# Performance work log

Hardware: AMD Instinct MI355X
Metric: run time of the kernel (lower is better)

The kernel has to match this reference:

```python
import jax, jax.numpy as jnp
import numpy as np
import math

B, N, D = 128, 64, 2
H, M, L = 64, 64, 2
OMEGA = 1.0


def setup_inputs() -> dict:
    key = jax.random.key(0)
    ks = jax.random.split(key, 32)
    s = 0.1  # param scale
    rn = lambda k, shp: jax.random.normal(k, shp, dtype=jnp.float32) * s
    inp = {
        "x": jax.random.normal(ks[0], (B, N, D), dtype=jnp.float32),
        "spin": jnp.zeros((B, N, 1), jnp.float32),
        "node_w1": rn(ks[1], (D + 1, H)), "node_b1": rn(ks[2], (H,)),
        "node_w2": rn(ks[3], (H, H)), "node_b2": rn(ks[4], (H,)),
        "edge_w1": rn(ks[5], (D + 2, M)), "edge_b1": rn(ks[6], (M,)),
        "edge_w2": rn(ks[7], (M, M)), "edge_b2": rn(ks[8], (M,)),
        "v2e_w1": rn(ks[9], (L, H + M, M)), "v2e_b1": rn(ks[10], (L, M)),
        "v2e_w2": rn(ks[11], (L, M, M)), "v2e_b2": rn(ks[12], (L, M)),
        "e2v_w1": rn(ks[13], (L, M, H)), "e2v_b1": rn(ks[14], (L, H)),
        "e2v_w2": rn(ks[15], (L, H, H)), "e2v_b2": rn(ks[16], (L, H)),
        "head_w1": rn(ks[17], (H, H)), "head_b1": rn(ks[18], (H,)),
        "head_w2": rn(ks[19], (H, D)), "head_b2": rn(ks[20], (D,)),
        # bf_scale_init=0.3 -> softplus-inverse
        "scale": jnp.array([math.log(math.exp(0.3) - 1.0)], jnp.float32),
    }
    return inp


def _mlp(x, w1, b1, w2, b2, act):
    return act(x @ w1 + b1) @ w2 + b2


def reference(x, spin, node_w1, node_b1, node_w2, node_b2,
              edge_w1, edge_b1, edge_w2, edge_b2,
              v2e_w1, v2e_b1, v2e_w2, v2e_b2,
              e2v_w1, e2v_b1, e2v_w2, e2v_b2,
              head_w1, head_b1, head_w2, head_b2, scale):
    gelu = lambda t: jax.nn.gelu(t, approximate=False)  # torch exact GELU
    b, n, d = x.shape
    xs = x * jnp.float32(math.sqrt(OMEGA))
    # node embedding: [B,N,H]
    hv = _mlp(jnp.concatenate([xs, spin], -1), node_w1, node_b1, node_w2, node_b2, gelu)
    # dense pairwise edge features; dr[b,i,j] = xs[b,j] - xs[b,i]
    dr = xs[:, None, :, :] - xs[:, :, None, :]            # [B,N,N,D]
    r2 = jnp.sum(dr * dr, axis=-1, keepdims=True)          # [B,N,N,1]
    rr = jnp.sqrt(r2 + 1e-12)
    he = _mlp(jnp.concatenate([dr, rr, r2], -1), edge_w1, edge_b1, edge_w2, edge_b2, gelu)  # [B,N,N,M]
    # mask excludes self-edges (i==j) from aggregation (they were never created
    # in the original edge list; their dense entries never influence off-diag values)
    mask = (1.0 - jnp.eye(n, dtype=x.dtype))[None, :, :, None]
    inv = jnp.float32(1.0 / max(n - 1, 1))
    for l in range(v2e_w1.shape[0]):
        hvb = jnp.broadcast_to(hv[:, :, None, :], (b, n, n, hv.shape[-1]))  # source node i
        he = _mlp(jnp.concatenate([hvb, he], -1), v2e_w1[l], v2e_b1[l], v2e_w2[l], v2e_b2[l], gelu)
        m = _mlp(he, e2v_w1[l], e2v_b1[l], e2v_w2[l], e2v_b2[l], gelu)      # [B,N,N,H]
        hv = hv + jnp.sum(m * mask, axis=1) * inv           # scatter-add over sources i into j
    dx = _mlp(hv, head_w1, head_b1, head_w2, head_b2, jnp.tanh) * jax.nn.softplus(scale[0])
    return dx - jnp.mean(dx, axis=1, keepdims=True)
```

## Files before the change

kernel.cpp:

```cpp
#include <hip/hip_runtime.h>
#include <math.h>


typedef unsigned short u16;
typedef unsigned int u32;
typedef _Float16 half8 __attribute__((ext_vector_type(8)));
typedef __attribute__((ext_vector_type(4))) float floatx4;

#define TS 72

__device__ __forceinline__ float gelu_f(float x) {
    float u = x * 0.70710678118654752f;
    float s = fabsf(u);
    float t = __builtin_amdgcn_rcpf(fmaf(0.3275911f, s, 1.0f));
    float P = t * fmaf(t, fmaf(t, fmaf(t, fmaf(t, 1.061405429f, -1.453152027f),
                                        1.421413741f), -0.284496736f), 0.254829592f);
    float r = copysignf(fmaf(-P, __expf(-s * s), 1.0f), u);
    return 0.5f * x * (1.0f + r);
}

__global__ __launch_bounds__(256) void k_pre1(
    const float* __restrict__ ew2, const float* __restrict__ w1he0,
    const float* __restrict__ w2_0, const float* __restrict__ u1_0,
    const float* __restrict__ w1he1, const float* __restrict__ w2_1,
    const float* __restrict__ u1_1,
    const float* __restrict__ eb2, const float* __restrict__ b2_0,
    const float* __restrict__ c1_0, const float* __restrict__ b2_1,
    const float* __restrict__ c1_1,
    const float* __restrict__ u2_0, const float* __restrict__ u2_1,
    const float* __restrict__ w1n, const float* __restrict__ hw1,
    _Float16* __restrict__ WF,
    float* __restrict__ biasA, float* __restrict__ biasB,
    float* __restrict__ biasC, float* __restrict__ biasD,
    float* __restrict__ u2_0T, float* __restrict__ u2_1T,
    float* __restrict__ w1nT, float* __restrict__ hw1T)
{
    int blk = blockIdx.x;
    if (blk < 64) {
        int s = blk >> 4;
        int idx = (blk & 15) * 256 + threadIdx.x;
        int k = idx >> 6, n = idx & 63;
        const float *A, *Bm;
        if (s == 0)      { A = ew2;  Bm = w1he0; }
        else if (s == 1) { A = w2_0; Bm = u1_0;  }
        else if (s == 2) { A = w2_0; Bm = w1he1; }
        else             { A = w2_1; Bm = u1_1;  }
        float acc = 0.f;
        for (int q = 0; q < 64; ++q) acc = fmaf(A[k * 64 + q], Bm[q * 64 + n], acc);
        int kc = k >> 5, qd = (k >> 3) & 3, jj = k & 7;
        WF[(((s * 2 + kc) * 64 + n) * 4 + qd) * 8 + jj] = (_Float16)acc;
    } else if (blk == 64) {
        int s = threadIdx.x >> 6, cc = threadIdx.x & 63;
        const float *bv, *Bm, *add; float* dst;
        if (s == 0)      { bv = eb2;  Bm = w1he0; add = nullptr; dst = biasA; }
        else if (s == 1) { bv = b2_0; Bm = u1_0;  add = c1_0;    dst = biasB; }
        else if (s == 2) { bv = b2_0; Bm = w1he1; add = nullptr; dst = biasC; }
        else             { bv = b2_1; Bm = u1_1;  add = c1_1;    dst = biasD; }
        float acc = add ? add[cc] : 0.f;
        for (int q = 0; q < 64; ++q) acc = fmaf(bv[q], Bm[q * 64 + cc], acc);
        dst[cc] = acc;
    } else {
        int idx = (blk - 65) * 256 + threadIdx.x;
        int s = idx >> 12, r = idx & 4095, m = r >> 6, tc = r & 63;
        const float* W = s == 0 ? u2_0 : s == 1 ? u2_1 : s == 2 ? w1n : hw1;
        float* WT      = s == 0 ? u2_0T : s == 1 ? u2_1T : s == 2 ? w1nT : hw1T;
        WT[tc * 64 + m] = W[m * 64 + tc];
    }
}

__global__ __launch_bounds__(256) void k_pre2(
    const float* __restrict__ x, const float* __restrict__ spin,
    const float* __restrict__ nw1, const float* __restrict__ nb1,
    const float* __restrict__ nw2, const float* __restrict__ nb2,
    const float* __restrict__ w1_0, const float* __restrict__ b1_0,
    const float* __restrict__ biasA,
    float* __restrict__ hv, float* __restrict__ p0)
{
    __shared__ float a[4][64];
    __shared__ float shv[4][64];
    int w = threadIdx.x >> 6, h = threadIdx.x & 63;
    int node = blockIdx.x * 4 + w;
    float2 xv = ((const float2*)x)[node];
    float sp = spin[node];
    float z = fmaf(xv.x, nw1[h], fmaf(xv.y, nw1[64 + h], fmaf(sp, nw1[128 + h], nb1[h])));
    a[w][h] = gelu_f(z);
    float acc = nb2[h];
    for (int k = 0; k < 64; ++k) acc = fmaf(a[w][k], nw2[k * 64 + h], acc);
    hv[node * 64 + h] = acc;
    shv[w][h] = acc;
    float pa = b1_0[h] + biasA[h];
    for (int k = 0; k < 64; ++k) pa = fmaf(shv[w][k], w1_0[k * 64 + h], pa);
    p0[node * 64 + h] = pa;
}

__device__ __forceinline__ void mfma_acc(
    const _Float16* __restrict__ tA, const _Float16* __restrict__ WF,
    int stage, int c, int quad, int nn, floatx4 acc[4])
{
    int sA = ((nn >> 2) & 3) << 3;
    #pragma unroll
    for (int kc = 0; kc < 2; ++kc) {
        half8 bf = *(const half8*)(WF + (((stage * 2 + kc) * 64 + c) * 4 + quad) * 8);
        int k0 = (kc * 32 + quad * 8) ^ sA;
        #pragma unroll
        for (int mt = 0; mt < 4; ++mt) {
            half8 af = *(const half8*)(tA + (mt * 16 + nn) * TS + k0);
            acc[mt] = __builtin_amdgcn_mfma_f32_16x16x32_f16(af, bf, acc[mt], 0, 0, 0);
        }
    }
}

__device__ __forceinline__ void init_bias(floatx4 acc[4], float bc) {
    #pragma unroll
    for (int mt = 0; mt < 4; ++mt) acc[mt] = (floatx4){bc, bc, bc, bc};
}
__device__ __forceinline__ void init_p(floatx4 acc[4], const float* __restrict__ p,
                                       int rowbase, int c, int quad) {
    #pragma unroll
    for (int mt = 0; mt < 4; ++mt)
        #pragma unroll
        for (int r = 0; r < 4; ++r)
            acc[mt][r] = p[(rowbase + mt * 16 + quad * 4 + r) * 64 + c];
}

__global__ __launch_bounds__(256, 8) void k_L0(
    const float* __restrict__ x,
    const float* __restrict__ ew1, const float* __restrict__ eb1,
    const float* __restrict__ p0,
    const float* __restrict__ biasB,
    const float* __restrict__ u2_0T, const float* __restrict__ c2_0,
    const _Float16* __restrict__ WF,
    const float* __restrict__ hv0, float* __restrict__ hv1,
    const float* __restrict__ w1nT, const float* __restrict__ b1n,
    const float* __restrict__ biasC,
    float* __restrict__ p1,
    u16* __restrict__ he0g)
{
    __shared__ __align__(16) _Float16 tA[64 * TS];
    __shared__ float sgeo[256];
    __shared__ float sS[64];
    __shared__ float shv[64];
    int t = threadIdx.x, w = t >> 6, L = t & 63;
    int nn = L & 15, quad = L >> 4;
    int c = w * 16 + nn;
    int cw = c ^ (quad << 3);
    int b = blockIdx.x >> 6, j = blockIdx.x & 63;

    if (t < 64) {
        float2 xi = ((const float2*)x)[b * 64 + t];
        float2 xj = ((const float2*)x)[b * 64 + j];
        float d0 = xj.x - xi.x, d1 = xj.y - xi.y;
        float r2 = fmaf(d0, d0, d1 * d1);
        sgeo[t] = d0; sgeo[64 + t] = d1; sgeo[128 + t] = sqrtf(r2 + 1e-12f); sgeo[192 + t] = r2;
    }
    __syncthreads();
    {
        int m = t & 63, i0 = t >> 6;
        float wa = ew1[m], wb = ew1[64 + m], wc = ew1[128 + m], wd = ew1[192 + m], bm = eb1[m];
        #pragma unroll
        for (int k = 0; k < 16; ++k) {
            int i = i0 + k * 4;
            float z = fmaf(sgeo[i], wa, fmaf(sgeo[64 + i], wb,
                      fmaf(sgeo[128 + i], wc, fmaf(sgeo[192 + i], wd, bm))));
            tA[i * TS + (m ^ (((i >> 2) & 3) << 3))] = (_Float16)gelu_f(z);
        }
    }
    __syncthreads();

    floatx4 acc[4];
    init_p(acc, p0, b * 64, c, quad);
    mfma_acc(tA, WF, 0, c, quad, nn, acc);
    __syncthreads();
    {
        u16* dst = he0g + (size_t)blockIdx.x * 4096;
        #pragma unroll
        for (int mt = 0; mt < 4; ++mt)
            #pragma unroll
            for (int r = 0; r < 4; ++r) {
                int i = mt * 16 + quad * 4 + r;
                _Float16 y = (_Float16)gelu_f(acc[mt][r]);
                tA[i * TS + cw] = y;
                dst[i * 64 + cw] = __builtin_bit_cast(u16, y);
            }
    }
    __syncthreads();
    init_bias(acc, biasB[c]);
    mfma_acc(tA, WF, 1, c, quad, nn, acc);
    {
        float s = 0.f;
        #pragma unroll
        for (int mt = 0; mt < 4; ++mt)
            #pragma unroll
            for (int r = 0; r < 4; ++r) {
                int i = mt * 16 + quad * 4 + r;
                float g = gelu_f(acc[mt][r]);
                s += (i == j) ? 0.f : g;
            }
        s += __shfl_xor(s, 16);
        s += __shfl_xor(s, 32);
        if (quad == 0) sS[c] = s;
    }
    __syncthreads();
    if (t < 64) {
        const float4* sv4 = (const float4*)sS;
        const float4* uv4 = (const float4*)(u2_0T + t * 64);
        float g = 0.f;
        #pragma unroll
        for (int m4 = 0; m4 < 16; ++m4) {
            float4 sv = sv4[m4], uv = uv4[m4];
            g = fmaf(sv.x, uv.x, fmaf(sv.y, uv.y, fmaf(sv.z, uv.z, fmaf(sv.w, uv.w, g))));
        }
        int o = blockIdx.x * 64 + t;
        float hvv = hv0[o] + g * (1.0f / 63.0f) + c2_0[t];
        hv1[o] = hvv;
        shv[t] = hvv;
        const float4* hv4 = (const float4*)shv;
        const float4* wv4 = (const float4*)(w1nT + t * 64);
        float pa = b1n[t] + biasC[t];
        #pragma unroll
        for (int m4 = 0; m4 < 16; ++m4) {
            float4 sv = hv4[m4], uv = wv4[m4];
            pa = fmaf(sv.x, uv.x, fmaf(sv.y, uv.y, fmaf(sv.z, uv.z, fmaf(sv.w, uv.w, pa))));
        }
        p1[o] = pa;
    }
}

__global__ __launch_bounds__(256, 8) void k_L1(
    const u16* __restrict__ he0g,
    const float* __restrict__ p1,
    const float* __restrict__ biasD,
    const float* __restrict__ u2_1T, const float* __restrict__ c2_1,
    const _Float16* __restrict__ WF,
    const float* __restrict__ hv1,
    const float* __restrict__ hw1T, const float* __restrict__ hb1,
    const float* __restrict__ hw2, const float* __restrict__ hb2,
    const float* __restrict__ scale, float* __restrict__ dx)
{
    __shared__ __align__(16) _Float16 tA[64 * TS];
    __shared__ float sS[64];
    __shared__ float shv[64];
    int t = threadIdx.x, w = t >> 6, L = t & 63;
    int nn = L & 15, quad = L >> 4;
    int c = w * 16 + nn;
    int cw = c ^ (quad << 3);
    int b = blockIdx.x >> 6, j = blockIdx.x & 63;

    {
        const u32* src = (const u32*)(he0g + (size_t)blockIdx.x * 4096);
        for (int qq = t; qq < 2048; qq += 256) {
            u32 v = src[qq];
            int i = qq >> 5, m2 = (qq & 31) * 2;
            *(u32*)((u16*)tA + i * TS + m2) = v;
        }
    }
    __syncthreads();

    floatx4 acc[4];
    init_p(acc, p1, b * 64, c, quad);
    mfma_acc(tA, WF, 2, c, quad, nn, acc);
    __syncthreads();
    #pragma unroll
    for (int mt = 0; mt < 4; ++mt)
        #pragma unroll
        for (int r = 0; r < 4; ++r)
            tA[(mt * 16 + quad * 4 + r) * TS + cw] = (_Float16)gelu_f(acc[mt][r]);
    __syncthreads();
    init_bias(acc, biasD[c]);
    mfma_acc(tA, WF, 3, c, quad, nn, acc);
    {
        float s = 0.f;
        #pragma unroll
        for (int mt = 0; mt < 4; ++mt)
            #pragma unroll
            for (int r = 0; r < 4; ++r) {
                int i = mt * 16 + quad * 4 + r;
                float g = gelu_f(acc[mt][r]);
                s += (i == j) ? 0.f : g;
            }
        s += __shfl_xor(s, 16);
        s += __shfl_xor(s, 32);
        if (quad == 0) sS[c] = s;
    }
    __syncthreads();
    if (t < 64) {
        const float4* sv4 = (const float4*)sS;
        const float4* uv4 = (const float4*)(u2_1T + t * 64);
        float g = 0.f;
        #pragma unroll
        for (int m4 = 0; m4 < 16; ++m4) {
            float4 sv = sv4[m4], uv = uv4[m4];
            g = fmaf(sv.x, uv.x, fmaf(sv.y, uv.y, fmaf(sv.z, uv.z, fmaf(sv.w, uv.w, g))));
        }
        float hv2 = hv1[blockIdx.x * 64 + t] + g * (1.0f / 63.0f) + c2_1[t];
        shv[t] = hv2;
        const float4* hv4 = (const float4*)shv;
        const float4* wv4 = (const float4*)(hw1T + t * 64);
        float a = hb1[t];
        #pragma unroll
        for (int m4 = 0; m4 < 16; ++m4) {
            float4 sv = hv4[m4], uv = wv4[m4];
            a = fmaf(sv.x, uv.x, fmaf(sv.y, uv.y, fmaf(sv.z, uv.z, fmaf(sv.w, uv.w, a))));
        }
        float t1 = tanhf(a);
        float d0 = t1 * hw2[t * 2], d1 = t1 * hw2[t * 2 + 1];
        #pragma unroll
        for (int off = 1; off <= 32; off <<= 1) { d0 += __shfl_xor(d0, off); d1 += __shfl_xor(d1, off); }
        if (t == 0) {
            float sp = log1pf(__expf(scale[0]));
            dx[blockIdx.x * 2 + 0] = (d0 + hb2[0]) * sp;
            dx[blockIdx.x * 2 + 1] = (d1 + hb2[1]) * sp;
        }
    }
}

__global__ __launch_bounds__(64) void k_mean(
    const float* __restrict__ dx, float* __restrict__ out)
{
    __shared__ float s0[64], s1[64];
    int b = blockIdx.x, j = threadIdx.x;
    float2 d = ((const float2*)dx)[b * 64 + j];
    s0[j] = d.x; s1[j] = d.y;
    __syncthreads();
    float m0 = 0.f, m1 = 0.f;
    for (int q = 0; q < 64; ++q) { m0 += s0[q]; m1 += s1[q]; }
    ((float2*)out)[b * 64 + j] = make_float2(d.x - m0 * (1.0f / 64.0f), d.y - m1 * (1.0f / 64.0f));
}

__global__ void k_beacon(float* out, float code) { out[0] = code; }

extern "C" void kernel_launch(void* const* d_in, const int* in_sizes, int n_in,
                              void* d_out, int out_size, void* d_ws, size_t ws_size,
                              hipStream_t stream)
{
    static const int exp_sizes[23] = {
        16384, 8192, 192, 64, 4096, 64,
        256, 64, 4096, 64,
        16384, 128, 8192, 128,
        8192, 128, 8192, 128,
        4096, 64, 128, 2, 1
    };
    float* hv0 = (float*)d_ws;
    float* hv1 = hv0 + 524288;
    float* p0  = hv1 + 524288;
    float* p1  = p0  + 524288;
    float* dx  = p1  + 524288;
    float* u2_0T = dx + 16384;
    float* u2_1T = u2_0T + 4096;
    float* w1nT  = u2_1T + 4096;
    float* hw1T  = w1nT + 4096;
    float* biasA = hw1T + 4096;
    float* biasB = biasA + 64;
    float* biasC = biasB + 64;
    float* biasD = biasC + 64;
    _Float16* WF = (_Float16*)(biasD + 64);
    u16* he0g  = (u16*)(WF + 16384);
    const size_t need = (size_t)((char*)(he0g + 33554432) - (char*)d_ws);

    int bad = -1;
    if (n_in != 23 || out_size != 16384) bad = 98;
    else if (ws_size < need) bad = 97;
    else for (int i = 0; i < 23; ++i)
        if (in_sizes[i] != exp_sizes[i]) { bad = i; break; }
    if (bad >= 0) {
        k_beacon<<<1, 1, 0, stream>>>((float*)d_out, 2e6f + bad * 1e4f);
        return;
    }

    const float* x      = (const float*)d_in[0];
    const float* spin   = (const float*)d_in[1];
    const float* nw1    = (const float*)d_in[2];
    const float* nb1    = (const float*)d_in[3];
    const float* nw2    = (const float*)d_in[4];
    const float* nb2    = (const float*)d_in[5];
    const float* ew1    = (const float*)d_in[6];
    const float* eb1    = (const float*)d_in[7];
    const float* ew2    = (const float*)d_in[8];
    const float* eb2    = (const float*)d_in[9];
    const float* v2e_w1 = (const float*)d_in[10];
    const float* v2e_b1 = (const float*)d_in[11];
    const float* v2e_w2 = (const float*)d_in[12];
    const float* v2e_b2 = (const float*)d_in[13];
    const float* e2v_w1 = (const float*)d_in[14];
    const float* e2v_b1 = (const float*)d_in[15];
    const float* e2v_w2 = (const float*)d_in[16];
    const float* e2v_b2 = (const float*)d_in[17];
    const float* hw1    = (const float*)d_in[18];
    const float* hb1    = (const float*)d_in[19];
    const float* hw2    = (const float*)d_in[20];
    const float* hb2    = (const float*)d_in[21];
    const float* scale  = (const float*)d_in[22];

    k_pre1<<<129, 256, 0, stream>>>(
        ew2, v2e_w1 + 4096, v2e_w2, e2v_w1,
        v2e_w1 + 12288, v2e_w2 + 4096, e2v_w1 + 4096,
        eb2, v2e_b2, e2v_b1, v2e_b2 + 64, e2v_b1 + 64,
        e2v_w2, e2v_w2 + 4096, v2e_w1 + 8192, hw1,
        WF, biasA, biasB, biasC, biasD,
        u2_0T, u2_1T, w1nT, hw1T);
    k_pre2<<<2048, 256, 0, stream>>>(x, spin, nw1, nb1, nw2, nb2,
                                     v2e_w1, v2e_b1, biasA, hv0, p0);
    k_L0<<<8192, 256, 0, stream>>>(x, ew1, eb1,
        p0, biasB, u2_0T, e2v_b2,
        WF, hv0, hv1,
        w1nT, v2e_b1 + 64, biasC, p1,
        he0g);
    k_L1<<<8192, 256, 0, stream>>>(he0g,
        p1, biasD, u2_1T, e2v_b2 + 64,
        WF, hv1, hw1T, hb1, hw2, hb2, scale, dx);
    k_mean<<<128, 64, 0, stream>>>(dx, (float*)d_out);
}
```

Before: 243.6 us.

## Use cheaper erf approximation, spread small matvecs across all waves, pad edge buffer

Swaps the 5-term Abramowitz-Stegun erf polynomial inside GELU for a 3-term version with lower accuracy. Spreads the per-block 64x64 matvecs (message aggregation, next-layer projection, head) across all four wavefronts with a shared-memory reduction, where only one wave did them before. Pads the fp16 edge intermediate to a 72-element row stride so k_L1 can copy it to LDS with 16-byte vector loads. Also builds the first edge-MLP layer per lane with packed half8 stores and no separate geometry staging pass, and folds v2e biases into the precomputed bias vectors. The cheaper erf adds error (about 2.5e-5 absolute), and the split matvecs add extra barriers.

```diff
diff --git a/kernel.cpp b/kernel.cpp
--- a/kernel.cpp
+++ b/kernel.cpp
@@ -8,13 +8,14 @@
 typedef __attribute__((ext_vector_type(4))) float floatx4;
 
 #define TS 72
+#define HROW 72
+#define HBLK (64 * HROW)
 
 __device__ __forceinline__ float gelu_f(float x) {
     float u = x * 0.70710678118654752f;
     float s = fabsf(u);
-    float t = __builtin_amdgcn_rcpf(fmaf(0.3275911f, s, 1.0f));
-    float P = t * fmaf(t, fmaf(t, fmaf(t, fmaf(t, 1.061405429f, -1.453152027f),
-                                        1.421413741f), -0.284496736f), 0.254829592f);
+    float t = __builtin_amdgcn_rcpf(fmaf(0.47047f, s, 1.0f));
+    float P = t * fmaf(t, fmaf(t, 0.7478556f, -0.0958798f), 0.3480242f);
     float r = copysignf(fmaf(-P, __expf(-s * s), 1.0f), u);
     return 0.5f * x * (1.0f + r);
 }
@@ -27,6 +28,7 @@
     const float* __restrict__ eb2, const float* __restrict__ b2_0,
     const float* __restrict__ c1_0, const float* __restrict__ b2_1,
     const float* __restrict__ c1_1,
+    const float* __restrict__ b1_0v, const float* __restrict__ b1nv,
     const float* __restrict__ u2_0, const float* __restrict__ u2_1,
     const float* __restrict__ w1n, const float* __restrict__ hw1,
     _Float16* __restrict__ WF,
@@ -52,11 +54,11 @@
     } else if (blk == 64) {
         int s = threadIdx.x >> 6, cc = threadIdx.x & 63;
         const float *bv, *Bm, *add; float* dst;
-        if (s == 0)      { bv = eb2;  Bm = w1he0; add = nullptr; dst = biasA; }
-        else if (s == 1) { bv = b2_0; Bm = u1_0;  add = c1_0;    dst = biasB; }
-        else if (s == 2) { bv = b2_0; Bm = w1he1; add = nullptr; dst = biasC; }
-        else             { bv = b2_1; Bm = u1_1;  add = c1_1;    dst = biasD; }
-        float acc = add ? add[cc] : 0.f;
+        if (s == 0)      { bv = eb2;  Bm = w1he0; add = b1_0v; dst = biasA; }
+        else if (s == 1) { bv = b2_0; Bm = u1_0;  add = c1_0;  dst = biasB; }
+        else if (s == 2) { bv = b2_0; Bm = w1he1; add = b1nv;  dst = biasC; }
+        else             { bv = b2_1; Bm = u1_1;  add = c1_1;  dst = biasD; }
+        float acc = add[cc];
         for (int q = 0; q < 64; ++q) acc = fmaf(bv[q], Bm[q * 64 + cc], acc);
         dst[cc] = acc;
     } else {
@@ -72,7 +74,7 @@
     const float* __restrict__ x, const float* __restrict__ spin,
     const float* __restrict__ nw1, const float* __restrict__ nb1,
     const float* __restrict__ nw2, const float* __restrict__ nb2,
-    const float* __restrict__ w1_0, const float* __restrict__ b1_0,
+    const float* __restrict__ w1_0,
     const float* __restrict__ biasA,
     float* __restrict__ hv, float* __restrict__ p0)
 {
@@ -88,7 +90,7 @@
     for (int k = 0; k < 64; ++k) acc = fmaf(a[w][k], nw2[k * 64 + h], acc);
     hv[node * 64 + h] = acc;
     shv[w][h] = acc;
-    float pa = b1_0[h] + biasA[h];
+    float pa = biasA[h];
     for (int k = 0; k < 64; ++k) pa = fmaf(shv[w][k], w1_0[k * 64 + h], pa);
     p0[node * 64 + h] = pa;
 }
@@ -131,39 +133,40 @@
     const float* __restrict__ u2_0T, const float* __restrict__ c2_0,
     const _Float16* __restrict__ WF,
     const float* __restrict__ hv0, float* __restrict__ hv1,
-    const float* __restrict__ w1nT, const float* __restrict__ b1n,
-    const float* __restrict__ biasC,
+    const float* __restrict__ w1nT, const float* __restrict__ biasC,
     float* __restrict__ p1,
     u16* __restrict__ he0g)
 {
     __shared__ __align__(16) _Float16 tA[64 * TS];
-    __shared__ float sgeo[256];
     __shared__ float sS[64];
     __shared__ float shv[64];
-    int t = threadIdx.x, w = t >> 6, L = t & 63;
+    __shared__ float sred[256];
+    int t = threadIdx.x, L = t & 63;
+    int w = __builtin_amdgcn_readfirstlane(t >> 6);
     int nn = L & 15, quad = L >> 4;
     int c = w * 16 + nn;
     int cw = c ^ (quad << 3);
     int b = blockIdx.x >> 6, j = blockIdx.x & 63;
 
-    if (t < 64) {
-        float2 xi = ((const float2*)x)[b * 64 + t];
-        float2 xj = ((const float2*)x)[b * 64 + j];
-        float d0 = xj.x - xi.x, d1 = xj.y - xi.y;
-        float r2 = fmaf(d0, d0, d1 * d1);
-        sgeo[t] = d0; sgeo[64 + t] = d1; sgeo[128 + t] = sqrtf(r2 + 1e-12f); sgeo[192 + t] = r2;
-    }
-    __syncthreads();
-    {
-        int m = t & 63, i0 = t >> 6;
-        float wa = ew1[m], wb = ew1[64 + m], wc = ew1[128 + m], wd = ew1[192 + m], bm = eb1[m];
-        #pragma unroll
-        for (int k = 0; k < 16; ++k) {
-            int i = i0 + k * 4;
-            float z = fmaf(sgeo[i], wa, fmaf(sgeo[64 + i], wb,
-                      fmaf(sgeo[128 + i], wc, fmaf(sgeo[192 + i], wd, bm))));
-            tA[i * TS + (m ^ (((i >> 2) & 3) << 3))] = (_Float16)gelu_f(z);
-        }
+    float2 xi = ((const float2*)x)[b * 64 + L];
+    float2 xj = ((const float2*)x)[b * 64 + j];
+    float d0 = xj.x - xi.x, d1 = xj.y - xi.y;
+    float r2 = fmaf(d0, d0, d1 * d1);
+    float rr = sqrtf(r2 + 1e-12f);
+    int swL = ((L >> 2) & 3) << 3;
+
+    #pragma unroll
+    for (int mb = 0; mb < 2; ++mb) {
+        int m0 = w * 16 + mb * 8;
+        half8 h8;
+        #pragma unroll
+        for (int kk = 0; kk < 8; ++kk) {
+            int m = m0 + kk;
+            float z = fmaf(d0, ew1[m], fmaf(d1, ew1[64 + m],
+                      fmaf(rr, ew1[128 + m], fmaf(r2, ew1[192 + m], eb1[m]))));
+            h8[kk] = (_Float16)gelu_f(z);
+        }
+        *(half8*)(tA + L * TS + (m0 ^ swL)) = h8;
     }
     __syncthreads();
 
@@ -172,7 +175,7 @@
     mfma_acc(tA, WF, 0, c, quad, nn, acc);
     __syncthreads();
     {
-        u16* dst = he0g + (size_t)blockIdx.x * 4096;
+        u16* dst = he0g + (size_t)blockIdx.x * HBLK;
         #pragma unroll
         for (int mt = 0; mt < 4; ++mt)
             #pragma unroll
@@ -180,7 +183,7 @@
                 int i = mt * 16 + quad * 4 + r;
                 _Float16 y = (_Float16)gelu_f(acc[mt][r]);
                 tA[i * TS + cw] = y;
-                dst[i * 64 + cw] = __builtin_bit_cast(u16, y);
+                dst[i * HROW + cw] = __builtin_bit_cast(u16, y);
             }
     }
     __syncthreads();
@@ -201,29 +204,40 @@
         if (quad == 0) sS[c] = s;
     }
     __syncthreads();
-    if (t < 64) {
-        const float4* sv4 = (const float4*)sS;
-        const float4* uv4 = (const float4*)(u2_0T + t * 64);
+    {
+        const float4* sv4 = (const float4*)(sS + w * 16);
+        const float4* uv4 = (const float4*)(u2_0T + L * 64 + w * 16);
         float g = 0.f;
         #pragma unroll
-        for (int m4 = 0; m4 < 16; ++m4) {
+        for (int m4 = 0; m4 < 4; ++m4) {
             float4 sv = sv4[m4], uv = uv4[m4];
             g = fmaf(sv.x, uv.x, fmaf(sv.y, uv.y, fmaf(sv.z, uv.z, fmaf(sv.w, uv.w, g))));
         }
+        sred[w * 64 + L] = g;
+    }
+    __syncthreads();
+    if (t < 64) {
+        float g = sred[t] + sred[64 + t] + sred[128 + t] + sred[192 + t];
         int o = blockIdx.x * 64 + t;
         float hvv = hv0[o] + g * (1.0f / 63.0f) + c2_0[t];
         hv1[o] = hvv;
         shv[t] = hvv;
-        const float4* hv4 = (const float4*)shv;
-        const float4* wv4 = (const float4*)(w1nT + t * 64);
-        float pa = b1n[t] + biasC[t];
-        #pragma unroll
-        for (int m4 = 0; m4 < 16; ++m4) {
+    }
+    __syncthreads();
+    {
+        const float4* hv4 = (const float4*)(shv + w * 16);
+        const float4* wv4 = (const float4*)(w1nT + L * 64 + w * 16);
+        float pa = 0.f;
+        #pragma unroll
+        for (int m4 = 0; m4 < 4; ++m4) {
             float4 sv = hv4[m4], uv = wv4[m4];
             pa = fmaf(sv.x, uv.x, fmaf(sv.y, uv.y, fmaf(sv.z, uv.z, fmaf(sv.w, uv.w, pa))));
         }
-        p1[o] = pa;
-    }
+        sred[w * 64 + L] = pa;
+    }
+    __syncthreads();
+    if (t < 64)
+        p1[blockIdx.x * 64 + t] = biasC[t] + sred[t] + sred[64 + t] + sred[128 + t] + sred[192 + t];
 }
 
 __global__ __launch_bounds__(256, 8) void k_L1(
@@ -240,19 +254,19 @@
     __shared__ __align__(16) _Float16 tA[64 * TS];
     __shared__ float sS[64];
     __shared__ float shv[64];
-    int t = threadIdx.x, w = t >> 6, L = t & 63;
+    __shared__ float sred[256];
+    int t = threadIdx.x, L = t & 63;
+    int w = __builtin_amdgcn_readfirstlane(t >> 6);
     int nn = L & 15, quad = L >> 4;
     int c = w * 16 + nn;
     int cw = c ^ (quad << 3);
     int b = blockIdx.x >> 6, j = blockIdx.x & 63;
 
     {
-        const u32* src = (const u32*)(he0g + (size_t)blockIdx.x * 4096);
-        for (int qq = t; qq < 2048; qq += 256) {
-            u32 v = src[qq];
-            int i = qq >> 5, m2 = (qq & 31) * 2;
-            *(u32*)((u16*)tA + i * TS + m2) = v;
-        }
+        const float4* src = (const float4*)(he0g + (size_t)blockIdx.x * HBLK);
+        float4* dstl = (float4*)tA;
+        for (int q = t; q < (HBLK * 2 / 16); q += 256)
+            dstl[q] = src[q];
     }
     __syncthreads();
 
@@ -283,33 +297,50 @@
         if (quad == 0) sS[c] = s;
     }
     __syncthreads();
-    if (t < 64) {
-        const float4* sv4 = (const float4*)sS;
-        const float4* uv4 = (const float4*)(u2_1T + t * 64);
+    {
+        const float4* sv4 = (const float4*)(sS + w * 16);
+        const float4* uv4 = (const float4*)(u2_1T + L * 64 + w * 16);
         float g = 0.f;
         #pragma unroll
-        for (int m4 = 0; m4 < 16; ++m4) {
+        for (int m4 = 0; m4 < 4; ++m4) {
             float4 sv = sv4[m4], uv = uv4[m4];
             g = fmaf(sv.x, uv.x, fmaf(sv.y, uv.y, fmaf(sv.z, uv.z, fmaf(sv.w, uv.w, g))));
         }
+        sred[w * 64 + L] = g;
+    }
+    __syncthreads();
+    if (t < 64) {
+        float g = sred[t] + sred[64 + t] + sred[128 + t] + sred[192 + t];
         float hv2 = hv1[blockIdx.x * 64 + t] + g * (1.0f / 63.0f) + c2_1[t];
         shv[t] = hv2;
-        const float4* hv4 = (const float4*)shv;
-        const float4* wv4 = (const float4*)(hw1T + t * 64);
-        float a = hb1[t];
-        #pragma unroll
-        for (int m4 = 0; m4 < 16; ++m4) {
+    }
+    __syncthreads();
+    {
+        const float4* hv4 = (const float4*)(shv + w * 16);
+        const float4* wv4 = (const float4*)(hw1T + L * 64 + w * 16);
+        float a = 0.f;
+        #pragma unroll
+        for (int m4 = 0; m4 < 4; ++m4) {
             float4 sv = hv4[m4], uv = wv4[m4];
             a = fmaf(sv.x, uv.x, fmaf(sv.y, uv.y, fmaf(sv.z, uv.z, fmaf(sv.w, uv.w, a))));
         }
-        float t1 = tanhf(a);
-        float d0 = t1 * hw2[t * 2], d1 = t1 * hw2[t * 2 + 1];
-        #pragma unroll
-        for (int off = 1; off <= 32; off <<= 1) { d0 += __shfl_xor(d0, off); d1 += __shfl_xor(d1, off); }
+        sred[w * 64 + L] = a;
+    }
+    __syncthreads();
+    if (t < 64) {
+        float a = hb1[t] + sred[t] + sred[64 + t] + sred[128 + t] + sred[192 + t];
+        sS[t] = tanhf(a);
+    }
+    __syncthreads();
+    if (t < 64) {
+        float t1 = sS[t];
+        float dd0 = t1 * hw2[t * 2], dd1 = t1 * hw2[t * 2 + 1];
+        #pragma unroll
+        for (int off = 1; off <= 32; off <<= 1) { dd0 += __shfl_xor(dd0, off); dd1 += __shfl_xor(dd1, off); }
         if (t == 0) {
             float sp = log1pf(__expf(scale[0]));
-            dx[blockIdx.x * 2 + 0] = (d0 + hb2[0]) * sp;
-            dx[blockIdx.x * 2 + 1] = (d1 + hb2[1]) * sp;
+            dx[blockIdx.x * 2 + 0] = (dd0 + hb2[0]) * sp;
+            dx[blockIdx.x * 2 + 1] = (dd1 + hb2[1]) * sp;
         }
     }
 }
@@ -355,7 +386,7 @@
     float* biasD = biasC + 64;
     _Float16* WF = (_Float16*)(biasD + 64);
     u16* he0g  = (u16*)(WF + 16384);
-    const size_t need = (size_t)((char*)(he0g + 33554432) - (char*)d_ws);
+    const size_t need = (size_t)((char*)(he0g + (size_t)8192 * HBLK) - (char*)d_ws);
 
     int bad = -1;
     if (n_in != 23 || out_size != 16384) bad = 98;
@@ -395,15 +426,16 @@
         ew2, v2e_w1 + 4096, v2e_w2, e2v_w1,
         v2e_w1 + 12288, v2e_w2 + 4096, e2v_w1 + 4096,
         eb2, v2e_b2, e2v_b1, v2e_b2 + 64, e2v_b1 + 64,
+        v2e_b1, v2e_b1 + 64,
         e2v_w2, e2v_w2 + 4096, v2e_w1 + 8192, hw1,
         WF, biasA, biasB, biasC, biasD,
         u2_0T, u2_1T, w1nT, hw1T);
     k_pre2<<<2048, 256, 0, stream>>>(x, spin, nw1, nb1, nw2, nb2,
-                                     v2e_w1, v2e_b1, biasA, hv0, p0);
+                                     v2e_w1, biasA, hv0, p0);
     k_L0<<<8192, 256, 0, stream>>>(x, ew1, eb1,
         p0, biasB, u2_0T, e2v_b2,
         WF, hv0, hv1,
-        w1nT, v2e_b1 + 64, biasC, p1,
+        w1nT, biasC, p1,
         he0g);
     k_L1<<<8192, 256, 0, stream>>>(he0g,
         p1, biasD, u2_1T, e2v_b2 + 64,
```

After: 227.3 us. -6.7%, faster.
